# Kernel tuning notes

Hardware: AMD Instinct MI355X
Metric: run time of the kernel (lower is better)

Reference implementation:

```python
import jax, jax.numpy as jnp
import numpy as np
from jax import lax

B, T, F = 8, 512, 128          # batch, mel time, mel freq
DM, DS, DC, EXP, NL = 384, 16, 4, 2, 12
DI = EXP * DM                   # 768 inner width
DTR = (DM + 15) // 16           # 24, mamba_ssm dt_rank='auto'
PT = PF = 16
L = (T // PT) * (F // PF)       # 256 patches
NC = 4


def setup_inputs() -> dict:
    key = jax.random.key(0)
    ks = iter(jax.random.split(key, 24))
    def n(shape, s=0.02):
        return jax.random.normal(next(ks), shape, jnp.float32) * s
    return {
        "x": jax.random.normal(next(ks), (B, T, F), jnp.float32),
        "patch_w": n((DM, PT, PF)),
        "patch_b": jnp.zeros((DM,), jnp.float32),
        "pos_embed": n((1, L, DM)),
        "ln_g": jnp.ones((NL, DM), jnp.float32),
        "ln_b": jnp.zeros((NL, DM), jnp.float32),
        "in_proj_w": n((NL, 2 * DI, DM)),
        "conv_w": n((NL, DI, DC), 0.1),
        "conv_b": jnp.zeros((NL, DI), jnp.float32),
        "x_proj_w": n((NL, DTR + 2 * DS, DI)),
        "dt_proj_w": n((NL, DI, DTR), 0.1),
        "dt_proj_b": n((NL, DI), 0.1),
        "A_log": jnp.tile(jnp.log(jnp.arange(1, DS + 1, dtype=jnp.float32))[None, None, :], (NL, DI, 1)),
        "Dskip": jnp.ones((NL, DI), jnp.float32),
        "out_proj_w": n((NL, DM, DI)),
        "fn_g": jnp.ones((DM,), jnp.float32),
        "fn_b": jnp.zeros((DM,), jnp.float32),
        "head_w": n((NC, DM)),
        "head_b": jnp.zeros((NC,), jnp.float32),
    }


def _layernorm(x, g, b):
    m = x.mean(-1, keepdims=True)
    v = jnp.var(x, axis=-1, keepdims=True)
    return (x - m) * lax.rsqrt(v + 1e-5) * g + b


def _silu(v):
    return v * jax.nn.sigmoid(v)


def _mamba_block(x, p):
    # x: [B, L, DM]; residual Mamba block (pre-LN, dropout=identity in eval)
    ln_g, ln_b, Wi, cw, cb, Wx, Wdt, bdt, A_log, Dsk, Wo = p
    res = x
    h = _layernorm(x, ln_g, ln_b)
    xz = jnp.einsum('bld,ed->ble', h, Wi)          # [B,L,2*DI]
    u, z = jnp.split(xz, 2, axis=-1)
    # causal depthwise conv1d, kernel DC (small, unrolled)
    up = jnp.pad(u, ((0, 0), (DC - 1, 0), (0, 0)))
    u = sum(up[:, k:k + L, :] * cw[:, k] for k in range(DC)) + cb
    u = _silu(u)
    proj = jnp.einsum('bld,ed->ble', u, Wx)        # [B,L,DTR+2*DS]
    dt, Bm, Cm = jnp.split(proj, [DTR, DTR + DS], axis=-1)
    delta = jax.nn.softplus(jnp.einsum('blr,dr->bld', dt, Wdt) + bdt)  # [B,L,DI]
    A = -jnp.exp(A_log)                            # [DI, DS]
    dA = jnp.exp(delta[..., None] * A)             # [B,L,DI,DS]
    dBu = (delta * u)[..., None] * Bm[:, :, None, :]

    def step(hst, inp):
        dA_t, dBu_t, C_t = inp
        hst = dA_t * hst + dBu_t                   # [B,DI,DS]
        return hst, jnp.einsum('bdn,bn->bd', hst, C_t)

    h0 = jnp.zeros((x.shape[0], DI, DS), x.dtype)
    _, ys = lax.scan(step, h0, (dA.swapaxes(0, 1), dBu.swapaxes(0, 1), Cm.swapaxes(0, 1)))
    y = ys.swapaxes(0, 1) + u * Dsk                # [B,L,DI]
    y = y * _silu(z)
    return res + jnp.einsum('bld,ed->ble', y, Wo)


def reference(x, patch_w, patch_b, pos_embed, ln_g, ln_b, in_proj_w, conv_w, conv_b,
              x_proj_w, dt_proj_w, dt_proj_b, A_log, Dskip, out_proj_w,
              fn_g, fn_b, head_w, head_b):
    Bn = x.shape[0]
    # patch embed = non-overlapping 16x16 conv == blocked reshape + einsum
    patches = x.reshape(Bn, T // PT, PT, F // PF, PF)
    tok = jnp.einsum('bhpwq,dpq->bhwd', patches, patch_w) + patch_b
    tok = tok.reshape(Bn, L, DM) + pos_embed

    def layer(carry, p):
        return _mamba_block(carry, p), None

    tok, _ = lax.scan(layer, tok, (ln_g, ln_b, in_proj_w, conv_w, conv_b,
                                   x_proj_w, dt_proj_w, dt_proj_b, A_log, Dskip, out_proj_w))
    tok = _layernorm(tok, fn_g, fn_b)
    pooled = tok.mean(axis=1)
    return pooled @ head_w.T + head_b
```

## Files before the change

kernel.cpp:

```cpp
#include <hip/hip_runtime.h>
#include <math.h>

namespace {

constexpr int kB   = 8;
constexpr int kL   = 256;
constexpr int kTok = 2048;
constexpr int kDM  = 384;
constexpr int kDI  = 768;
constexpr int kDS  = 16;
constexpr int kDTR = 24;
constexpr int kPROJ = 56;
constexpr int kNL  = 12;

constexpr int kWIN  = 2 * kDI * kDM;
constexpr int kWOUT = kDM * kDI;
constexpr int kWX   = kPROJ * kDI;
constexpr int kWTOT = kWIN + kWOUT + kWX;

typedef float f32x4 __attribute__((ext_vector_type(4)));
typedef short short8 __attribute__((ext_vector_type(8)));

__device__ __forceinline__ float softplus_f(float x) {
  return (x > 20.f) ? x : log1pf(__expf(x));
}
__device__ __forceinline__ float silu_f(float x) {
  return x / (1.f + __expf(-x));
}
__device__ __forceinline__ unsigned short f2bf(float f) {
  union { float f; unsigned u; } v; v.f = f;
  unsigned r = v.u + 0x7FFFu + ((v.u >> 16) & 1u);
  return (unsigned short)(r >> 16);
}
__device__ __forceinline__ float bf2f(unsigned short u) {
  return __uint_as_float((unsigned)u << 16);
}

__global__ __launch_bounds__(256) void patch_gemm_k(
    const float* __restrict__ x, const float* __restrict__ Bw,
    const float* __restrict__ bias, const float* __restrict__ pos,
    float* __restrict__ C) {
  __shared__ float As[16][68];
  __shared__ float Bs[16][68];
  int tid = threadIdx.x;
  int bm = blockIdx.y * 64;
  int bn = blockIdx.x * 64;
  int lr = tid >> 2;
  int lk = (tid & 3) << 2;
  int tm = (tid >> 4) << 2;
  int tn = (tid & 15) << 2;
  float acc[4][4] = {};
  for (int k0 = 0; k0 < 256; k0 += 16) {
    {
      int token = bm + lr;
      int b = token >> 8, l = token & 255;
      int h = l >> 3, w = l & 7;
      int p = k0 >> 4;
      const float* ap = x + ((size_t)(b * 512) + h * 16 + p) * 128 + w * 16 + lk;
      float4 av = *(const float4*)ap;
      As[lk + 0][lr] = av.x; As[lk + 1][lr] = av.y;
      As[lk + 2][lr] = av.z; As[lk + 3][lr] = av.w;
    }
    {
      const float* bp = Bw + (size_t)(bn + lr) * 256 + k0 + lk;
      float4 bv = *(const float4*)bp;
      Bs[lk + 0][lr] = bv.x; Bs[lk + 1][lr] = bv.y;
      Bs[lk + 2][lr] = bv.z; Bs[lk + 3][lr] = bv.w;
    }
    __syncthreads();
    #pragma unroll
    for (int k = 0; k < 16; ++k) {
      float4 a = *(const float4*)&As[k][tm];
      float4 b = *(const float4*)&Bs[k][tn];
      float av[4] = {a.x, a.y, a.z, a.w};
      float bv[4] = {b.x, b.y, b.z, b.w};
      #pragma unroll
      for (int i = 0; i < 4; ++i)
        #pragma unroll
        for (int j = 0; j < 4; ++j)
          acc[i][j] = fmaf(av[i], bv[j], acc[i][j]);
    }
    __syncthreads();
  }
  #pragma unroll
  for (int i = 0; i < 4; ++i) {
    int row = bm + tm + i;
    #pragma unroll
    for (int j = 0; j < 4; ++j) {
      int col = bn + tn + j;
      C[(size_t)row * kDM + col] =
          acc[i][j] + bias[col] + pos[(size_t)(row & 255) * kDM + col];
    }
  }
}

__global__ __launch_bounds__(384) void lnpool_k(
    const float* __restrict__ in, float* __restrict__ pooled,
    const float* __restrict__ g, const float* __restrict__ bb) {
  int t = blockIdx.x, d = threadIdx.x;
  float v = in[(size_t)t * kDM + d];
  float s = v, s2 = v * v;
  #pragma unroll
  for (int m = 32; m >= 1; m >>= 1) {
    s  += __shfl_xor(s, m);
    s2 += __shfl_xor(s2, m);
  }
  __shared__ float ps[6], ps2[6];
  if ((d & 63) == 0) { ps[d >> 6] = s; ps2[d >> 6] = s2; }
  __syncthreads();
  float S = 0.f, S2 = 0.f;
  #pragma unroll
  for (int i = 0; i < 6; ++i) { S += ps[i]; S2 += ps2[i]; }
  float mean = S * (1.f / 384.f);
  float var  = S2 * (1.f / 384.f) - mean * mean;
  float r = rsqrtf(var + 1e-5f);
  float o = (v - mean) * r * g[d] + bb[d];
  atomicAdd(&pooled[(size_t)(t >> 8) * kDM + d], o * (1.f / 256.f));
}

__global__ __launch_bounds__(256) void convert_all_k(
    const float* __restrict__ w_in, const float* __restrict__ w_out,
    const float* __restrict__ w_x, unsigned short* __restrict__ dst,
    float* __restrict__ pooled_zero) {
  int layer = blockIdx.y;
  int tid = threadIdx.x;
  if (layer == 0 && blockIdx.x == 0) {
    for (int i = tid; i < kB * kDM; i += 256) pooled_zero[i] = 0.f;
  }
  int i4 = (blockIdx.x * 256 + tid) * 4;
  if (i4 >= kWTOT) return;
  const float* src;
  int off;
  if (i4 < kWIN) { src = w_in + (size_t)layer * kWIN; off = i4; }
  else if (i4 < kWIN + kWOUT) { src = w_out + (size_t)layer * kWOUT; off = i4 - kWIN; }
  else { src = w_x + (size_t)layer * kWX; off = i4 - kWIN - kWOUT; }
  float4 v = *(const float4*)(src + off);
  unsigned short o[4] = {f2bf(v.x), f2bf(v.y), f2bf(v.z), f2bf(v.w)};
  *(uint2*)(dst + (size_t)layer * kWTOT + i4) = *(const uint2*)o;
}

__global__ __launch_bounds__(256) void inproj_ln_k(
    const float* __restrict__ tok, const unsigned short* __restrict__ Bw,
    const float* __restrict__ g, const float* __restrict__ bb,
    unsigned short* __restrict__ Cbf, float* __restrict__ proj_zero) {
  __shared__ __align__(16) unsigned short As[4][64][8];
  __shared__ __align__(16) unsigned short Bs[4][128][8];
  __shared__ float smean[64], srstd[64];
  __shared__ float sg_[kDM], sb_[kDM];
  int tid = threadIdx.x;
  int bm = blockIdx.y * 64;
  int bn = blockIdx.x * 128;
  {
    int bid = blockIdx.y * 12 + blockIdx.x;
    for (int i = bid * 256 + tid; i < kTok * kPROJ; i += 384 * 256)
      proj_zero[i] = 0.f;
  }
  for (int i = tid; i < kDM; i += 256) { sg_[i] = g[i]; sb_[i] = bb[i]; }
  {
    int r = tid >> 2, quarter = tid & 3;
    const float* rp = tok + (size_t)(bm + r) * kDM + quarter * 96;
    float s = 0.f, s2 = 0.f;
    #pragma unroll
    for (int q = 0; q < 24; ++q) {
      float4 v = ((const float4*)rp)[q];
      s  += v.x + v.y + v.z + v.w;
      s2 += v.x * v.x + v.y * v.y + v.z * v.z + v.w * v.w;
    }
    s  += __shfl_xor(s, 1);  s2 += __shfl_xor(s2, 1);
    s  += __shfl_xor(s, 2);  s2 += __shfl_xor(s2, 2);
    if (quarter == 0) {
      float mean = s * (1.f / 384.f);
      float var  = s2 * (1.f / 384.f) - mean * mean;
      smean[r] = mean;
      srstd[r] = rsqrtf(var + 1e-5f);
    }
  }
  __syncthreads();
  int wave = tid >> 6, lane = tid & 63;
  int lm = lane & 15, lq = lane >> 4;
  int wm = (wave & 1) * 32, wn = (wave >> 1) * 64;
  f32x4 acc[2][4] = {};
  for (int k0 = 0; k0 < kDM; k0 += 32) {
    int ar = tid & 63, aq = tid >> 6;
    unsigned short av[8];
    {
      float mean = smean[ar], rstd = srstd[ar];
      const float* ap = tok + (size_t)(bm + ar) * kDM + k0 + aq * 8;
      float4 v0 = ((const float4*)ap)[0];
      float4 v1 = ((const float4*)ap)[1];
      float vv[8] = {v0.x, v0.y, v0.z, v0.w, v1.x, v1.y, v1.z, v1.w};
      #pragma unroll
      for (int j = 0; j < 8; ++j) {
        int k = k0 + aq * 8 + j;
        av[j] = f2bf((vv[j] - mean) * rstd * sg_[k] + sb_[k]);
      }
    }
    int br = tid & 127, bq0 = tid >> 7, bq1 = bq0 + 2;
    uint4 b0 = *(const uint4*)(Bw + (size_t)(bn + br) * kDM + k0 + bq0 * 8);
    uint4 b1 = *(const uint4*)(Bw + (size_t)(bn + br) * kDM + k0 + bq1 * 8);
    __syncthreads();
    *(uint4*)&As[aq][ar][0]  = *(const uint4*)av;
    *(uint4*)&Bs[bq0][br][0] = b0;
    *(uint4*)&Bs[bq1][br][0] = b1;
    __syncthreads();
    short8 bfrag[4];
    #pragma unroll
    for (int ni = 0; ni < 4; ++ni)
      bfrag[ni] = *(const short8*)&Bs[lq][wn + ni * 16 + lm][0];
    #pragma unroll
    for (int mi = 0; mi < 2; ++mi) {
      short8 afrag = *(const short8*)&As[lq][wm + mi * 16 + lm][0];
      #pragma unroll
      for (int ni = 0; ni < 4; ++ni)
        acc[mi][ni] = __builtin_amdgcn_mfma_f32_16x16x32_bf16(
            afrag, bfrag[ni], acc[mi][ni], 0, 0, 0);
    }
  }
  #pragma unroll
  for (int mi = 0; mi < 2; ++mi) {
    #pragma unroll
    for (int ni = 0; ni < 4; ++ni) {
      int grow0 = bm + wm + mi * 16 + lq * 4;
      int gcol = bn + wn + ni * 16 + lm;
      #pragma unroll
      for (int r = 0; r < 4; ++r)
        Cbf[(size_t)(grow0 + r) * (2 * kDI) + gcol] = f2bf(acc[mi][ni][r]);
    }
  }
}

__global__ __launch_bounds__(256) void xproj_conv_k(
    const unsigned short* __restrict__ xz, const unsigned short* __restrict__ Bw,
    const float* __restrict__ cw, const float* __restrict__ cb,
    float* __restrict__ proj, unsigned short* __restrict__ uT_bf,
    unsigned short* __restrict__ sgT_bf) {
  __shared__ __align__(16) unsigned short As[4][64][8];
  __shared__ __align__(16) unsigned short Bs[4][64][8];
  __shared__ float scw[128][4];
  __shared__ float scb[128];
  int tid = threadIdx.x;
  int bm = blockIdx.x * 64;
  int kbase = blockIdx.y * 128;
  int wave = tid >> 6, lane = tid & 63;
  int lm = lane & 15, lq = lane >> 4;
  int wm = wave * 16;
  f32x4 acc[4] = {};

  if (tid < 128) {
    *(float4*)&scw[tid][0] = *(const float4*)(cw + (size_t)(kbase + tid) * 4);
    scb[tid] = cb[kbase + tid];
  }
  __syncthreads();

  int ar = tid & 63;
  int aq = tid >> 6;
  int t = bm + ar;
  int b = t >> 8, l = t & 255;

  for (int kt = 0; kt < 4; ++kt) {
    int k0 = kbase + kt * 32;
    int dloc = kt * 32 + aq * 8;
    int dg = kbase + dloc;
    unsigned short av[8];
    {
      float vals[4][8];
      #pragma unroll
      for (int q = 0; q < 4; ++q) {
        if (l - 3 + q >= 0) {
          uint4 r = *(const uint4*)(xz + (size_t)(t - 3 + q) * (2 * kDI) + dg);
          const unsigned short* rs = (const unsigned short*)&r;
          #pragma unroll
          for (int j = 0; j < 8; ++j) vals[q][j] = bf2f(rs[j]);
        } else {
          #pragma unroll
          for (int j = 0; j < 8; ++j) vals[q][j] = 0.f;
        }
      }
      uint4 zr = *(const uint4*)(xz + (size_t)t * (2 * kDI) + kDI + dg);
      const unsigned short* zs = (const unsigned short*)&zr;
      #pragma unroll
      for (int j = 0; j < 8; ++j) {
        float a = scb[dloc + j];
        a = fmaf(vals[0][j], scw[dloc + j][0], a);
        a = fmaf(vals[1][j], scw[dloc + j][1], a);
        a = fmaf(vals[2][j], scw[dloc + j][2], a);
        a = fmaf(vals[3][j], scw[dloc + j][3], a);
        unsigned short ub = f2bf(silu_f(a));
        av[j] = ub;
        size_t rbase = ((size_t)b * kDI + dg + j) * kL + l;
        uT_bf[rbase] = ub;
        sgT_bf[rbase] = f2bf(silu_f(bf2f(zs[j])));
      }
    }
    int br = tid & 63, bq = tid >> 6;
    uint4 b0;
    if (br < kPROJ)
      b0 = *(const uint4*)(Bw + (size_t)br * kDI + k0 + bq * 8);
    else
      b0 = make_uint4(0u, 0u, 0u, 0u);
    __syncthreads();
    *(uint4*)&As[aq][ar][0] = *(const uint4*)av;
    *(uint4*)&Bs[bq][br][0] = b0;
    __syncthreads();
    short8 afrag = *(const short8*)&As[lq][wm + lm][0];
    #pragma unroll
    for (int ni = 0; ni < 4; ++ni) {
      short8 bfrag = *(const short8*)&Bs[lq][ni * 16 + lm][0];
      acc[ni] = __builtin_amdgcn_mfma_f32_16x16x32_bf16(
          afrag, bfrag, acc[ni], 0, 0, 0);
    }
  }

  #pragma unroll
  for (int ni = 0; ni < 4; ++ni) {
    int grow0 = bm + wm + lq * 4;
    int gcol = ni * 16 + lm;
    if (gcol < kPROJ) {
      #pragma unroll
      for (int r = 0; r < 4; ++r)
        atomicAdd(&proj[(size_t)(grow0 + r) * kPROJ + gcol], acc[ni][r]);
    }
  }
}

__global__ __launch_bounds__(256) void bgemm_out_k(
    const unsigned short* __restrict__ A, int lda,
    const unsigned short* __restrict__ B, int ldb,
    float* __restrict__ C, int ldc, int Kc) {
  __shared__ __align__(16) unsigned short As[4][64][8];
  __shared__ __align__(16) unsigned short Bs[4][64][8];
  int tid = threadIdx.x;
  int bm = blockIdx.y * 64;
  int bn = blockIdx.x * 64;
  int k_begin = blockIdx.z * Kc;
  int wave = tid >> 6, lane = tid & 63;
  int lm = lane & 15, lq = lane >> 4;
  int wm = (wave & 1) * 32, wn = (wave >> 1) * 32;
  f32x4 acc[2][2] = {};

  for (int kt = 0; kt < Kc; kt += 32) {
    int k0 = k_begin + kt;
    int ar = tid & 63, aq = tid >> 6;
    uint4 a0 = *(const uint4*)(A + (size_t)(bm + ar) * lda + k0 + aq * 8);
    uint4 b0 = *(const uint4*)(B + (size_t)(bn + ar) * ldb + k0 + aq * 8);
    __syncthreads();
    *(uint4*)&As[aq][ar][0] = a0;
    *(uint4*)&Bs[aq][ar][0] = b0;
    __syncthreads();
    short8 bfrag[2];
    #pragma unroll
    for (int ni = 0; ni < 2; ++ni)
      bfrag[ni] = *(const short8*)&Bs[lq][wn + ni * 16 + lm][0];
    #pragma unroll
    for (int mi = 0; mi < 2; ++mi) {
      short8 afrag = *(const short8*)&As[lq][wm + mi * 16 + lm][0];
      #pragma unroll
      for (int ni = 0; ni < 2; ++ni)
        acc[mi][ni] = __builtin_amdgcn_mfma_f32_16x16x32_bf16(
            afrag, bfrag[ni], acc[mi][ni], 0, 0, 0);
    }
  }

  #pragma unroll
  for (int mi = 0; mi < 2; ++mi) {
    #pragma unroll
    for (int ni = 0; ni < 2; ++ni) {
      int grow0 = bm + wm + mi * 16 + lq * 4;
      int gcol = bn + wn + ni * 16 + lm;
      #pragma unroll
      for (int r = 0; r < 4; ++r)
        atomicAdd(&C[(size_t)(grow0 + r) * ldc + gcol], acc[mi][ni][r]);
    }
  }
}

__global__ __launch_bounds__(256, 3) void scansplit_k(
    const float* __restrict__ proj, const unsigned short* __restrict__ uT_bf,
    const unsigned short* __restrict__ sgT_bf, const float* __restrict__ dtw,
    const float* __restrict__ dtb, const float* __restrict__ A_log,
    const float* __restrict__ Dsk, unsigned short* __restrict__ y_bf) {
  int d0 = blockIdx.x * 4;
  int b = blockIdx.y;
  int tid = threadIdx.x;
  int dsub = tid & 3;
  int nq = (tid >> 2) & 3;
  int c = tid >> 4;
  int d = d0 + dsub;
  __shared__ float sproj[256][33];
  __shared__ float sdt[16][16][5];
  __shared__ float sh[16][16][5];
  __shared__ float sca[16][16][5];

  const float* pr0 = proj + (size_t)(b * kL) * kPROJ;

  {
    const float* rp = pr0 + (size_t)tid * kPROJ;
    #pragma unroll
    for (int q = 0; q < 6; ++q) {
      float4 v = ((const float4*)rp)[q];
      sproj[tid][q * 4 + 0] = v.x;
      sproj[tid][q * 4 + 1] = v.y;
      sproj[tid][q * 4 + 2] = v.z;
      sproj[tid][q * 4 + 3] = v.w;
    }
  }

  float Av2[4];
  {
    const float kLog2e = 1.44269504088896340736f;
    float4 v = *(const float4*)(A_log + (size_t)d * kDS + nq * 4);
    Av2[0] = -__expf(v.x) * kLog2e;
    Av2[1] = -__expf(v.y) * kLog2e;
    Av2[2] = -__expf(v.z) * kLog2e;
    Av2[3] = -__expf(v.w) * kLog2e;
  }
  float bdt = dtb[d];
  float Dv = Dsk[d];

  float wdt[24];
  {
    const float* wp = dtw + (size_t)d * kDTR;
    #pragma unroll
    for (int q = 0; q < 6; ++q) {
      float4 v = ((const float4*)wp)[q];
      wdt[q * 4 + 0] = v.x; wdt[q * 4 + 1] = v.y;
      wdt[q * 4 + 2] = v.z; wdt[q * 4 + 3] = v.w;
    }
  }

  union { uint4 v[2]; unsigned short s[16]; } uu;
  {
    const unsigned short* up = uT_bf + ((size_t)b * kDI + d) * kL + c * 16;
    uu.v[0] = ((const uint4*)up)[0];
    uu.v[1] = ((const uint4*)up)[1];
  }

  __syncthreads();

  #pragma unroll
  for (int i = 0; i < 4; ++i) {
    int tok = c * 16 + nq * 4 + i;
    float acc = bdt;
    #pragma unroll
    for (int r = 0; r < 24; ++r) acc = fmaf(sproj[tok][r], wdt[r], acc);
    sdt[c][nq * 4 + i][dsub] = softplus_f(acc);
  }
  __syncthreads();

  {
    const float* rp = pr0 + (size_t)tid * kPROJ + 24;
    #pragma unroll
    for (int q = 0; q < 8; ++q) {
      float4 v = ((const float4*)rp)[q];
      sproj[tid][q * 4 + 0] = v.x;
      sproj[tid][q * 4 + 1] = v.y;
      sproj[tid][q * 4 + 2] = v.z;
      sproj[tid][q * 4 + 3] = v.w;
    }
  }
  __syncthreads();

  float h[4] = {};
  float S = 0.f;
  #pragma unroll
  for (int i = 0; i < 16; ++i) {
    int tok = c * 16 + i;
    float dl = sdt[c][i][dsub];
    float du = dl * bf2f(uu.s[i]);
    S += dl;
    #pragma unroll
    for (int n = 0; n < 4; ++n) {
      float a = exp2f(dl * Av2[n]);
      h[n] = fmaf(a, h[n], du * sproj[tok][nq * 4 + n]);
    }
  }
  {
    int nrow = nq * 4;
    #pragma unroll
    for (int n = 0; n < 4; ++n) {
      sh[c][nrow + n][dsub] = h[n];
      sca[c][nrow + n][dsub] = exp2f(S * Av2[n]);
    }
  }
  __syncthreads();

  float h0[4] = {};
  {
    int nrow = nq * 4;
    for (int j = 0; j < c; ++j) {
      #pragma unroll
      for (int n = 0; n < 4; ++n)
        h0[n] = fmaf(sca[j][nrow + n][dsub], h0[n], sh[j][nrow + n][dsub]);
    }
  }

  union { uint4 v[2]; unsigned short s[16]; } zz;
  zz.v[0] = make_uint4(0u, 0u, 0u, 0u);
  zz.v[1] = make_uint4(0u, 0u, 0u, 0u);
  if (nq == 0) {
    const unsigned short* sp = sgT_bf + ((size_t)b * kDI + d) * kL + c * 16;
    zz.v[0] = ((const uint4*)sp)[0];
    zz.v[1] = ((const uint4*)sp)[1];
  }

  unsigned short* yp = y_bf + (size_t)(b * kL + c * 16) * kDI + d;
  #pragma unroll
  for (int i = 0; i < 16; ++i) {
    int tok = c * 16 + i;
    float dl = sdt[c][i][dsub];
    float uv = bf2f(uu.s[i]);
    float du = dl * uv;
    float yv = 0.f;
    #pragma unroll
    for (int n = 0; n < 4; ++n) {
      float a = exp2f(dl * Av2[n]);
      h0[n] = fmaf(a, h0[n], du * sproj[tok][nq * 4 + n]);
      yv = fmaf(h0[n], sproj[tok][16 + nq * 4 + n], yv);
    }
    yv += __shfl_xor(yv, 4);
    yv += __shfl_xor(yv, 8);
    if (nq == 0) yp[(size_t)i * kDI] = f2bf((yv + uv * Dv) * bf2f(zz.s[i]));
  }
}

__global__ __launch_bounds__(64) void head_k(
    const float* __restrict__ pooled, const float* __restrict__ hw,
    const float* __restrict__ hb, float* __restrict__ out) {
  int b = blockIdx.x >> 2, c = blockIdx.x & 3;
  int lane = threadIdx.x;
  float acc = 0.f;
  for (int dd = lane; dd < kDM; dd += 64)
    acc = fmaf(pooled[b * kDM + dd], hw[c * kDM + dd], acc);
  #pragma unroll
  for (int m = 32; m >= 1; m >>= 1) acc += __shfl_xor(acc, m);
  if (lane == 0) out[b * 4 + c] = acc + hb[c];
}

}

extern "C" void kernel_launch(void* const* d_in, const int* in_sizes, int n_in,
                              void* d_out, int out_size, void* d_ws, size_t ws_size,
                              hipStream_t stream) {
  (void)in_sizes; (void)n_in; (void)out_size; (void)ws_size;
  const float* x        = (const float*)d_in[0];
  const float* patch_w  = (const float*)d_in[1];
  const float* patch_b  = (const float*)d_in[2];
  const float* pos      = (const float*)d_in[3];
  const float* ln_g     = (const float*)d_in[4];
  const float* ln_b     = (const float*)d_in[5];
  const float* in_w     = (const float*)d_in[6];
  const float* conv_w   = (const float*)d_in[7];
  const float* conv_b   = (const float*)d_in[8];
  const float* xproj_w  = (const float*)d_in[9];
  const float* dtproj_w = (const float*)d_in[10];
  const float* dtproj_b = (const float*)d_in[11];
  const float* A_log    = (const float*)d_in[12];
  const float* Dskip    = (const float*)d_in[13];
  const float* out_w    = (const float*)d_in[14];
  const float* fn_g     = (const float*)d_in[15];
  const float* fn_b     = (const float*)d_in[16];
  const float* head_w   = (const float*)d_in[17];
  const float* head_b   = (const float*)d_in[18];
  float* out = (float*)d_out;

  float* ws = (float*)d_ws;
  float* tok    = ws; ws += kTok * kDM;
  float* proj   = ws; ws += kTok * kPROJ;
  float* pooled = ws; ws += kB * kDM;
  unsigned short* xz_bf  = (unsigned short*)ws; ws += kTok * 2 * kDI / 2;
  unsigned short* uT_bf  = (unsigned short*)ws; ws += kTok * kDI / 2;
  unsigned short* sgT_bf = (unsigned short*)ws; ws += kTok * kDI / 2;
  unsigned short* y_bf   = (unsigned short*)ws; ws += kTok * kDI / 2;
  unsigned short* w_bf   = (unsigned short*)ws; ws += (size_t)kNL * kWTOT / 2;

  convert_all_k<<<dim3(kWTOT / 4 / 256, kNL), 256, 0, stream>>>(
      in_w, out_w, xproj_w, w_bf, pooled);

  patch_gemm_k<<<dim3(6, 32), 256, 0, stream>>>(x, patch_w, patch_b, pos, tok);

  for (int layer = 0; layer < kNL; ++layer) {
    const unsigned short* wl = w_bf + (size_t)layer * kWTOT;
    inproj_ln_k<<<dim3(12, 32), 256, 0, stream>>>(
        tok, wl, ln_g + layer * kDM, ln_b + layer * kDM, xz_bf, proj);
    xproj_conv_k<<<dim3(32, 6), 256, 0, stream>>>(
        xz_bf, wl + kWIN + kWOUT, conv_w + layer * kDI * 4,
        conv_b + layer * kDI, proj, uT_bf, sgT_bf);
    scansplit_k<<<dim3(kDI / 4, kB), 256, 0, stream>>>(
        proj, uT_bf, sgT_bf, dtproj_w + (size_t)layer * kDI * kDTR,
        dtproj_b + layer * kDI, A_log + (size_t)layer * kDI * kDS,
        Dskip + layer * kDI, y_bf);
    bgemm_out_k<<<dim3(6, 32, 4), 256, 0, stream>>>(
        y_bf, kDI, wl + kWIN, kDI, tok, kDM, kDI / 4);
  }

  lnpool_k<<<kTok, kDM, 0, stream>>>(tok, pooled, fn_g, fn_b);
  head_k<<<kB * 4, 64, 0, stream>>>(pooled, head_w, head_b, out);
}
```

Before: 1.164 ms.

## Fuse all layers into one persistent kernel with software grid barriers

Replaces the roughly fifty per-layer kernel launches with a single persistent mega kernel sized to two blocks per CU. Blocks loop over work units for each stage and synchronise through an atomic counter grid barrier. The in-projection tile also changes from 128 to 96 columns to produce more work units. This is meant to remove launch overhead and inter-kernel gaps, at the cost of barrier spin time, reduced occupancy from the shared 48KB scratch, and a deadlock risk if not all blocks are co-resident.

```diff
diff --git a/kernel.cpp b/kernel.cpp
--- a/kernel.cpp
+++ b/kernel.cpp
@@ -36,96 +36,27 @@
   return __uint_as_float((unsigned)u << 16);
 }
 
-__global__ __launch_bounds__(256) void patch_gemm_k(
-    const float* __restrict__ x, const float* __restrict__ Bw,
-    const float* __restrict__ bias, const float* __restrict__ pos,
-    float* __restrict__ C) {
-  __shared__ float As[16][68];
-  __shared__ float Bs[16][68];
-  int tid = threadIdx.x;
-  int bm = blockIdx.y * 64;
-  int bn = blockIdx.x * 64;
-  int lr = tid >> 2;
-  int lk = (tid & 3) << 2;
-  int tm = (tid >> 4) << 2;
-  int tn = (tid & 15) << 2;
-  float acc[4][4] = {};
-  for (int k0 = 0; k0 < 256; k0 += 16) {
-    {
-      int token = bm + lr;
-      int b = token >> 8, l = token & 255;
-      int h = l >> 3, w = l & 7;
-      int p = k0 >> 4;
-      const float* ap = x + ((size_t)(b * 512) + h * 16 + p) * 128 + w * 16 + lk;
-      float4 av = *(const float4*)ap;
-      As[lk + 0][lr] = av.x; As[lk + 1][lr] = av.y;
-      As[lk + 2][lr] = av.z; As[lk + 3][lr] = av.w;
-    }
-    {
-      const float* bp = Bw + (size_t)(bn + lr) * 256 + k0 + lk;
-      float4 bv = *(const float4*)bp;
-      Bs[lk + 0][lr] = bv.x; Bs[lk + 1][lr] = bv.y;
-      Bs[lk + 2][lr] = bv.z; Bs[lk + 3][lr] = bv.w;
-    }
-    __syncthreads();
-    #pragma unroll
-    for (int k = 0; k < 16; ++k) {
-      float4 a = *(const float4*)&As[k][tm];
-      float4 b = *(const float4*)&Bs[k][tn];
-      float av[4] = {a.x, a.y, a.z, a.w};
-      float bv[4] = {b.x, b.y, b.z, b.w};
-      #pragma unroll
-      for (int i = 0; i < 4; ++i)
-        #pragma unroll
-        for (int j = 0; j < 4; ++j)
-          acc[i][j] = fmaf(av[i], bv[j], acc[i][j]);
-    }
-    __syncthreads();
+__device__ __forceinline__ void gbar(unsigned* cnt, unsigned target) {
+  __syncthreads();
+  if (threadIdx.x == 0) {
+    __builtin_amdgcn_fence(__ATOMIC_SEQ_CST, "agent");
+    __hip_atomic_fetch_add(cnt, 1u, __ATOMIC_RELAXED, __HIP_MEMORY_SCOPE_AGENT);
+    while (__hip_atomic_load(cnt, __ATOMIC_RELAXED, __HIP_MEMORY_SCOPE_AGENT) < target)
+      __builtin_amdgcn_s_sleep(2);
+    __builtin_amdgcn_fence(__ATOMIC_SEQ_CST, "agent");
   }
-  #pragma unroll
-  for (int i = 0; i < 4; ++i) {
-    int row = bm + tm + i;
-    #pragma unroll
-    for (int j = 0; j < 4; ++j) {
-      int col = bn + tn + j;
-      C[(size_t)row * kDM + col] =
-          acc[i][j] + bias[col] + pos[(size_t)(row & 255) * kDM + col];
-    }
-  }
-}
-
-__global__ __launch_bounds__(384) void lnpool_k(
-    const float* __restrict__ in, float* __restrict__ pooled,
-    const float* __restrict__ g, const float* __restrict__ bb) {
-  int t = blockIdx.x, d = threadIdx.x;
-  float v = in[(size_t)t * kDM + d];
-  float s = v, s2 = v * v;
-  #pragma unroll
-  for (int m = 32; m >= 1; m >>= 1) {
-    s  += __shfl_xor(s, m);
-    s2 += __shfl_xor(s2, m);
-  }
-  __shared__ float ps[6], ps2[6];
-  if ((d & 63) == 0) { ps[d >> 6] = s; ps2[d >> 6] = s2; }
   __syncthreads();
-  float S = 0.f, S2 = 0.f;
-  #pragma unroll
-  for (int i = 0; i < 6; ++i) { S += ps[i]; S2 += ps2[i]; }
-  float mean = S * (1.f / 384.f);
-  float var  = S2 * (1.f / 384.f) - mean * mean;
-  float r = rsqrtf(var + 1e-5f);
-  float o = (v - mean) * r * g[d] + bb[d];
-  atomicAdd(&pooled[(size_t)(t >> 8) * kDM + d], o * (1.f / 256.f));
 }
 
 __global__ __launch_bounds__(256) void convert_all_k(
     const float* __restrict__ w_in, const float* __restrict__ w_out,
     const float* __restrict__ w_x, unsigned short* __restrict__ dst,
-    float* __restrict__ pooled_zero) {
+    float* __restrict__ pooled_zero, unsigned* __restrict__ bar) {
   int layer = blockIdx.y;
   int tid = threadIdx.x;
   if (layer == 0 && blockIdx.x == 0) {
     for (int i = tid; i < kB * kDM; i += 256) pooled_zero[i] = 0.f;
+    if (tid < 64) bar[tid] = 0u;
   }
   int i4 = (blockIdx.x * 256 + tid) * 4;
   if (i4 >= kWTOT) return;
@@ -139,401 +70,506 @@
   *(uint2*)(dst + (size_t)layer * kWTOT + i4) = *(const uint2*)o;
 }
 
-__global__ __launch_bounds__(256) void inproj_ln_k(
-    const float* __restrict__ tok, const unsigned short* __restrict__ Bw,
-    const float* __restrict__ g, const float* __restrict__ bb,
-    unsigned short* __restrict__ Cbf, float* __restrict__ proj_zero) {
-  __shared__ __align__(16) unsigned short As[4][64][8];
-  __shared__ __align__(16) unsigned short Bs[4][128][8];
-  __shared__ float smean[64], srstd[64];
-  __shared__ float sg_[kDM], sb_[kDM];
-  int tid = threadIdx.x;
-  int bm = blockIdx.y * 64;
-  int bn = blockIdx.x * 128;
+__global__ __launch_bounds__(256, 2) void mega_k(
+    const float* __restrict__ x, const float* __restrict__ patch_w,
+    const float* __restrict__ patch_b, const float* __restrict__ pos,
+    float* __restrict__ tok,
+    const float* __restrict__ ln_g, const float* __restrict__ ln_b,
+    const unsigned short* __restrict__ w_bf,
+    const float* __restrict__ conv_w, const float* __restrict__ conv_b,
+    const float* __restrict__ dtw_all, const float* __restrict__ dtb_all,
+    const float* __restrict__ Alog_all, const float* __restrict__ Dsk_all,
+    float* __restrict__ proj, unsigned short* __restrict__ xz_bf,
+    unsigned short* __restrict__ uT_bf, unsigned short* __restrict__ sgT_bf,
+    unsigned short* __restrict__ y_bf,
+    const float* __restrict__ fn_g, const float* __restrict__ fn_b,
+    const float* __restrict__ head_w, const float* __restrict__ head_b,
+    float* __restrict__ pooled, float* __restrict__ out,
+    unsigned* __restrict__ bar, int nblk) {
+  __shared__ __align__(16) char smem[49152];
+  const int tid = threadIdx.x;
+  const int bid = blockIdx.x;
+  const int wave = tid >> 6, lane = tid & 63;
+  unsigned bt = 0;
+
   {
-    int bid = blockIdx.y * 12 + blockIdx.x;
-    for (int i = bid * 256 + tid; i < kTok * kPROJ; i += 384 * 256)
-      proj_zero[i] = 0.f;
+    float (*As)[68] = (float(*)[68])smem;
+    float (*Bs)[68] = (float(*)[68])(smem + 4352);
+    for (int u = bid; u < 192; u += nblk) {
+      __syncthreads();
+      int bm = (u / 6) * 64;
+      int bn = (u % 6) * 64;
+      int lr = tid >> 2;
+      int lk = (tid & 3) << 2;
+      int tm = (tid >> 4) << 2;
+      int tn = (tid & 15) << 2;
+      float acc[4][4] = {};
+      for (int k0 = 0; k0 < 256; k0 += 16) {
+        {
+          int token = bm + lr;
+          int b = token >> 8, l = token & 255;
+          int h = l >> 3, w = l & 7;
+          int p = k0 >> 4;
+          const float* ap = x + ((size_t)(b * 512) + h * 16 + p) * 128 + w * 16 + lk;
+          float4 av = *(const float4*)ap;
+          As[lk + 0][lr] = av.x; As[lk + 1][lr] = av.y;
+          As[lk + 2][lr] = av.z; As[lk + 3][lr] = av.w;
+        }
+        {
+          const float* bp = patch_w + (size_t)(bn + lr) * 256 + k0 + lk;
+          float4 bv = *(const float4*)bp;
+          Bs[lk + 0][lr] = bv.x; Bs[lk + 1][lr] = bv.y;
+          Bs[lk + 2][lr] = bv.z; Bs[lk + 3][lr] = bv.w;
+        }
+        __syncthreads();
+        #pragma unroll
+        for (int k = 0; k < 16; ++k) {
+          float4 a = *(const float4*)&As[k][tm];
+          float4 b = *(const float4*)&Bs[k][tn];
+          float av[4] = {a.x, a.y, a.z, a.w};
+          float bv[4] = {b.x, b.y, b.z, b.w};
+          #pragma unroll
+          for (int i = 0; i < 4; ++i)
+            #pragma unroll
+            for (int j = 0; j < 4; ++j)
+              acc[i][j] = fmaf(av[i], bv[j], acc[i][j]);
+        }
+        __syncthreads();
+      }
+      #pragma unroll
+      for (int i = 0; i < 4; ++i) {
+        int row = bm + tm + i;
+        #pragma unroll
+        for (int j = 0; j < 4; ++j) {
+          int col = bn + tn + j;
+          tok[(size_t)row * kDM + col] =
+              acc[i][j] + patch_b[col] + pos[(size_t)(row & 255) * kDM + col];
+        }
+      }
+    }
   }
-  for (int i = tid; i < kDM; i += 256) { sg_[i] = g[i]; sb_[i] = bb[i]; }
+  gbar(bar, bt += (unsigned)nblk);
+
+  for (int layer = 0; layer < kNL; ++layer) {
+    const unsigned short* wl = w_bf + (size_t)layer * kWTOT;
+
+    {
+      for (int i = bid * 256 + tid; i < kTok * kPROJ; i += nblk * 256)
+        proj[i] = 0.f;
+      float* sg_ = (float*)smem;
+      float* sb_ = (float*)(smem + 1536);
+      float* smean = (float*)(smem + 3072);
+      float* srstd = (float*)(smem + 3328);
+      auto As = (unsigned short (*)[64][8])(smem + 3584);
+      auto Bs = (unsigned short (*)[96][8])(smem + 7680);
+      const float* g = ln_g + (size_t)layer * kDM;
+      const float* bbp = ln_b + (size_t)layer * kDM;
+      for (int u = bid; u < 512; u += nblk) {
+        __syncthreads();
+        int bm = (u >> 4) * 64;
+        int bn = (u & 15) * 96;
+        for (int i = tid; i < kDM; i += 256) { sg_[i] = g[i]; sb_[i] = bbp[i]; }
+        {
+          int r = tid >> 2, quarter = tid & 3;
+          const float* rp = tok + (size_t)(bm + r) * kDM + quarter * 96;
+          float s = 0.f, s2 = 0.f;
+          #pragma unroll
+          for (int q = 0; q < 24; ++q) {
+            float4 v = ((const float4*)rp)[q];
+            s  += v.x + v.y + v.z + v.w;
+            s2 += v.x * v.x + v.y * v.y + v.z * v.z + v.w * v.w;
+          }
+          s  += __shfl_xor(s, 1);  s2 += __shfl_xor(s2, 1);
+          s  += __shfl_xor(s, 2);  s2 += __shfl_xor(s2, 2);
+          if (quarter == 0) {
+            float mean = s * (1.f / 384.f);
+            float var  = s2 * (1.f / 384.f) - mean * mean;
+            smean[r] = mean;
+            srstd[r] = rsqrtf(var + 1e-5f);
+          }
+        }
+        __syncthreads();
+        int lm = lane & 15, lq = lane >> 4;
+        int wm = (wave & 1) * 32, wn = (wave >> 1) * 48;
+        int ar = tid & 63, aq = tid >> 6;
+        int r0 = tid >> 2, q0 = tid & 3;
+        int r1 = (tid + 256) >> 2;
+        f32x4 acc[2][3] = {};
+        for (int k0 = 0; k0 < kDM; k0 += 32) {
+          unsigned short av[8];
+          {
+            float mean = smean[ar], rstd = srstd[ar];
+            const float* ap = tok + (size_t)(bm + ar) * kDM + k0 + aq * 8;
+            float4 v0 = ((const float4*)ap)[0];
+            float4 v1 = ((const float4*)ap)[1];
+            float vv[8] = {v0.x, v0.y, v0.z, v0.w, v1.x, v1.y, v1.z, v1.w};
+            #pragma unroll
+            for (int j = 0; j < 8; ++j) {
+              int k = k0 + aq * 8 + j;
+              av[j] = f2bf((vv[j] - mean) * rstd * sg_[k] + sb_[k]);
+            }
+          }
+          uint4 bv0 = *(const uint4*)(wl + (size_t)(bn + r0) * kDM + k0 + q0 * 8);
+          uint4 bv1 = make_uint4(0u, 0u, 0u, 0u);
+          if (tid < 128)
+            bv1 = *(const uint4*)(wl + (size_t)(bn + r1) * kDM + k0 + q0 * 8);
+          __syncthreads();
+          *(uint4*)&As[aq][ar][0] = *(const uint4*)av;
+          *(uint4*)&Bs[q0][r0][0] = bv0;
+          if (tid < 128) *(uint4*)&Bs[q0][r1][0] = bv1;
+          __syncthreads();
+          short8 bfrag[3];
+          #pragma unroll
+          for (int ni = 0; ni < 3; ++ni)
+            bfrag[ni] = *(const short8*)&Bs[lq][wn + ni * 16 + lm][0];
+          #pragma unroll
+          for (int mi = 0; mi < 2; ++mi) {
+            short8 afrag = *(const short8*)&As[lq][wm + mi * 16 + lm][0];
+            #pragma unroll
+            for (int ni = 0; ni < 3; ++ni)
+              acc[mi][ni] = __builtin_amdgcn_mfma_f32_16x16x32_bf16(
+                  afrag, bfrag[ni], acc[mi][ni], 0, 0, 0);
+          }
+        }
+        #pragma unroll
+        for (int mi = 0; mi < 2; ++mi) {
+          #pragma unroll
+          for (int ni = 0; ni < 3; ++ni) {
+            int grow0 = bm + wm + mi * 16 + lq * 4;
+            int gcol = bn + wn + ni * 16 + lm;
+            #pragma unroll
+            for (int r = 0; r < 4; ++r)
+              xz_bf[(size_t)(grow0 + r) * (2 * kDI) + gcol] = f2bf(acc[mi][ni][r]);
+          }
+        }
+      }
+    }
+    gbar(bar, bt += (unsigned)nblk);
+
+    {
+      auto As = (unsigned short (*)[64][8])smem;
+      auto Bs = (unsigned short (*)[64][8])(smem + 4096);
+      auto scw = (float (*)[4])(smem + 8192);
+      float* scb = (float*)(smem + 10240);
+      const float* cw = conv_w + (size_t)layer * kDI * 4;
+      const float* cb = conv_b + (size_t)layer * kDI;
+      const unsigned short* Bw = wl + kWIN + kWOUT;
+      for (int u = bid; u < 192; u += nblk) {
+        __syncthreads();
+        int bm = (u & 31) * 64;
+        int kbase = (u >> 5) * 128;
+        int lm = lane & 15, lq = lane >> 4;
+        int wm = wave * 16;
+        f32x4 acc[4] = {};
+        if (tid < 128) {
+          *(float4*)&scw[tid][0] = *(const float4*)(cw + (size_t)(kbase + tid) * 4);
+          scb[tid] = cb[kbase + tid];
+        }
+        __syncthreads();
+        int ar = tid & 63;
+        int aq = tid >> 6;
+        int t = bm + ar;
+        int b = t >> 8, l = t & 255;
+        for (int kt = 0; kt < 4; ++kt) {
+          int k0 = kbase + kt * 32;
+          int dloc = kt * 32 + aq * 8;
+          int dg = kbase + dloc;
+          unsigned short av[8];
+          {
+            float vals[4][8];
+            #pragma unroll
+            for (int q = 0; q < 4; ++q) {
+              if (l - 3 + q >= 0) {
+                uint4 r = *(const uint4*)(xz_bf + (size_t)(t - 3 + q) * (2 * kDI) + dg);
+                const unsigned short* rs = (const unsigned short*)&r;
+                #pragma unroll
+                for (int j = 0; j < 8; ++j) vals[q][j] = bf2f(rs[j]);
+              } else {
+                #pragma unroll
+                for (int j = 0; j < 8; ++j) vals[q][j] = 0.f;
+              }
+            }
+            uint4 zr = *(const uint4*)(xz_bf + (size_t)t * (2 * kDI) + kDI + dg);
+            const unsigned short* zs = (const unsigned short*)&zr;
+            #pragma unroll
+            for (int j = 0; j < 8; ++j) {
+              float a = scb[dloc + j];
+              a = fmaf(vals[0][j], scw[dloc + j][0], a);
+              a = fmaf(vals[1][j], scw[dloc + j][1], a);
+              a = fmaf(vals[2][j], scw[dloc + j][2], a);
+              a = fmaf(vals[3][j], scw[dloc + j][3], a);
+              unsigned short ub = f2bf(silu_f(a));
+              av[j] = ub;
+              size_t rbase = ((size_t)b * kDI + dg + j) * kL + l;
+              uT_bf[rbase] = ub;
+              sgT_bf[rbase] = f2bf(silu_f(bf2f(zs[j])));
+            }
+          }
+          int br = tid & 63, bq = tid >> 6;
+          uint4 b0;
+          if (br < kPROJ)
+            b0 = *(const uint4*)(Bw + (size_t)br * kDI + k0 + bq * 8);
+          else
+            b0 = make_uint4(0u, 0u, 0u, 0u);
+          __syncthreads();
+          *(uint4*)&As[aq][ar][0] = *(const uint4*)av;
+          *(uint4*)&Bs[bq][br][0] = b0;
+          __syncthreads();
+          short8 afrag = *(const short8*)&As[lq][wm + lm][0];
+          #pragma unroll
+          for (int ni = 0; ni < 4; ++ni) {
+            short8 bfrag = *(const short8*)&Bs[lq][ni * 16 + lm][0];
+            acc[ni] = __builtin_amdgcn_mfma_f32_16x16x32_bf16(
+                afrag, bfrag, acc[ni], 0, 0, 0);
+          }
+        }
+        #pragma unroll
+        for (int ni = 0; ni < 4; ++ni) {
+          int grow0 = bm + wm + lq * 4;
+          int gcol = ni * 16 + lm;
+          if (gcol < kPROJ) {
+            #pragma unroll
+            for (int r = 0; r < 4; ++r)
+              atomicAdd(&proj[(size_t)(grow0 + r) * kPROJ + gcol], acc[ni][r]);
+          }
+        }
+      }
+    }
+    gbar(bar, bt += (unsigned)nblk);
+
+    {
+      float (*sproj)[33] = (float(*)[33])smem;
+      auto sdt = (float (*)[16][5])(smem + 33792);
+      auto sh  = (float (*)[16][5])(smem + 38912);
+      auto sca = (float (*)[16][5])(smem + 44032);
+      const float* dtw = dtw_all + (size_t)layer * kDI * kDTR;
+      const float* dtb = dtb_all + (size_t)layer * kDI;
+      const float* Alog = Alog_all + (size_t)layer * kDI * kDS;
+      const float* Dskp = Dsk_all + (size_t)layer * kDI;
+      int dsub = tid & 3;
+      int nq = (tid >> 2) & 3;
+      int c = tid >> 4;
+      for (int u = bid; u < 1536; u += nblk) {
+        __syncthreads();
+        int d0 = (u % 192) * 4;
+        int b = u / 192;
+        int d = d0 + dsub;
+        const float* pr0 = proj + (size_t)(b * kL) * kPROJ;
+        {
+          const float* rp = pr0 + (size_t)tid * kPROJ;
+          #pragma unroll
+          for (int q = 0; q < 6; ++q) {
+            float4 v = ((const float4*)rp)[q];
+            sproj[tid][q * 4 + 0] = v.x;
+            sproj[tid][q * 4 + 1] = v.y;
+            sproj[tid][q * 4 + 2] = v.z;
+            sproj[tid][q * 4 + 3] = v.w;
+          }
+        }
+        float Av2[4];
+        {
+          const float kLog2e = 1.44269504088896340736f;
+          float4 v = *(const float4*)(Alog + (size_t)d * kDS + nq * 4);
+          Av2[0] = -__expf(v.x) * kLog2e;
+          Av2[1] = -__expf(v.y) * kLog2e;
+          Av2[2] = -__expf(v.z) * kLog2e;
+          Av2[3] = -__expf(v.w) * kLog2e;
+        }
+        float bdt = dtb[d];
+        float Dv = Dskp[d];
+        float wdt[24];
+        {
+          const float* wp = dtw + (size_t)d * kDTR;
+          #pragma unroll
+          for (int q = 0; q < 6; ++q) {
+            float4 v = ((const float4*)wp)[q];
+            wdt[q * 4 + 0] = v.x; wdt[q * 4 + 1] = v.y;
+            wdt[q * 4 + 2] = v.z; wdt[q * 4 + 3] = v.w;
+          }
+        }
+        union { uint4 v[2]; unsigned short s[16]; } uu;
+        {
+          const unsigned short* up = uT_bf + ((size_t)b * kDI + d) * kL + c * 16;
+          uu.v[0] = ((const uint4*)up)[0];
+          uu.v[1] = ((const uint4*)up)[1];
+        }
+        __syncthreads();
+        #pragma unroll
+        for (int i = 0; i < 4; ++i) {
+          int tk = c * 16 + nq * 4 + i;
+          float acc = bdt;
+          #pragma unroll
+          for (int r = 0; r < 24; ++r) acc = fmaf(sproj[tk][r], wdt[r], acc);
+          sdt[c][nq * 4 + i][dsub] = softplus_f(acc);
+        }
+        __syncthreads();
+        {
+          const float* rp = pr0 + (size_t)tid * kPROJ + 24;
+          #pragma unroll
+          for (int q = 0; q < 8; ++q) {
+            float4 v = ((const float4*)rp)[q];
+            sproj[tid][q * 4 + 0] = v.x;
+            sproj[tid][q * 4 + 1] = v.y;
+            sproj[tid][q * 4 + 2] = v.z;
+            sproj[tid][q * 4 + 3] = v.w;
+          }
+        }
+        __syncthreads();
+        float h[4] = {};
+        float S = 0.f;
+        #pragma unroll
+        for (int i = 0; i < 16; ++i) {
+          int tk = c * 16 + i;
+          float dl = sdt[c][i][dsub];
+          float du = dl * bf2f(uu.s[i]);
+          S += dl;
+          #pragma unroll
+          for (int n = 0; n < 4; ++n) {
+            float a = exp2f(dl * Av2[n]);
+            h[n] = fmaf(a, h[n], du * sproj[tk][nq * 4 + n]);
+          }
+        }
+        {
+          int nrow = nq * 4;
+          #pragma unroll
+          for (int n = 0; n < 4; ++n) {
+            sh[c][nrow + n][dsub] = h[n];
+            sca[c][nrow + n][dsub] = exp2f(S * Av2[n]);
+          }
+        }
+        __syncthreads();
+        float h0[4] = {};
+        {
+          int nrow = nq * 4;
+          for (int j = 0; j < c; ++j) {
+            #pragma unroll
+            for (int n = 0; n < 4; ++n)
+              h0[n] = fmaf(sca[j][nrow + n][dsub], h0[n], sh[j][nrow + n][dsub]);
+          }
+        }
+        union { uint4 v[2]; unsigned short s[16]; } zz;
+        zz.v[0] = make_uint4(0u, 0u, 0u, 0u);
+        zz.v[1] = make_uint4(0u, 0u, 0u, 0u);
+        if (nq == 0) {
+          const unsigned short* sp = sgT_bf + ((size_t)b * kDI + d) * kL + c * 16;
+          zz.v[0] = ((const uint4*)sp)[0];
+          zz.v[1] = ((const uint4*)sp)[1];
+        }
+        unsigned short* yp = y_bf + (size_t)(b * kL + c * 16) * kDI + d;
+        #pragma unroll
+        for (int i = 0; i < 16; ++i) {
+          int tk = c * 16 + i;
+          float dl = sdt[c][i][dsub];
+          float uv = bf2f(uu.s[i]);
+          float du = dl * uv;
+          float yv = 0.f;
+          #pragma unroll
+          for (int n = 0; n < 4; ++n) {
+            float a = exp2f(dl * Av2[n]);
+            h0[n] = fmaf(a, h0[n], du * sproj[tk][nq * 4 + n]);
+            yv = fmaf(h0[n], sproj[tk][16 + nq * 4 + n], yv);
+          }
+          yv += __shfl_xor(yv, 4);
+          yv += __shfl_xor(yv, 8);
+          if (nq == 0) yp[(size_t)i * kDI] = f2bf((yv + uv * Dv) * bf2f(zz.s[i]));
+        }
+      }
+    }
+    gbar(bar, bt += (unsigned)nblk);
+
+    {
+      auto As = (unsigned short (*)[64][8])smem;
+      auto Bs = (unsigned short (*)[64][8])(smem + 4096);
+      const unsigned short* Bw = wl + kWIN;
+      for (int u = bid; u < 768; u += nblk) {
+        __syncthreads();
+        int bn = (u % 6) * 64;
+        int bm = ((u / 6) & 31) * 64;
+        int k_begin = (u / 192) * 192;
+        int lm = lane & 15, lq = lane >> 4;
+        int wm = (wave & 1) * 32, wn = (wave >> 1) * 32;
+        f32x4 acc[2][2] = {};
+        for (int kt = 0; kt < 192; kt += 32) {
+          int k0 = k_begin + kt;
+          int ar = tid & 63, aq = tid >> 6;
+          uint4 a0 = *(const uint4*)(y_bf + (size_t)(bm + ar) * kDI + k0 + aq * 8);
+          uint4 b0 = *(const uint4*)(Bw + (size_t)(bn + ar) * kDI + k0 + aq * 8);
+          __syncthreads();
+          *(uint4*)&As[aq][ar][0] = a0;
+          *(uint4*)&Bs[aq][ar][0] = b0;
+          __syncthreads();
+          short8 bfrag[2];
+          #pragma unroll
+          for (int ni = 0; ni < 2; ++ni)
+            bfrag[ni] = *(const short8*)&Bs[lq][wn + ni * 16 + lm][0];
+          #pragma unroll
+          for (int mi = 0; mi < 2; ++mi) {
+            short8 afrag = *(const short8*)&As[lq][wm + mi * 16 + lm][0];
+            #pragma unroll
+            for (int ni = 0; ni < 2; ++ni)
+              acc[mi][ni] = __builtin_amdgcn_mfma_f32_16x16x32_bf16(
+                  afrag, bfrag[ni], acc[mi][ni], 0, 0, 0);
+          }
+        }
+        #pragma unroll
+        for (int mi = 0; mi < 2; ++mi) {
+          #pragma unroll
+          for (int ni = 0; ni < 2; ++ni) {
+            int grow0 = bm + wm + mi * 16 + lq * 4;
+            int gcol = bn + wn + ni * 16 + lm;
+            #pragma unroll
+            for (int r = 0; r < 4; ++r)
+              atomicAdd(&tok[(size_t)(grow0 + r) * kDM + gcol], acc[mi][ni][r]);
+          }
+        }
+      }
+    }
+    gbar(bar, bt += (unsigned)nblk);
+  }
+
   {
-    int r = tid >> 2, quarter = tid & 3;
-    const float* rp = tok + (size_t)(bm + r) * kDM + quarter * 96;
-    float s = 0.f, s2 = 0.f;
-    #pragma unroll
-    for (int q = 0; q < 24; ++q) {
-      float4 v = ((const float4*)rp)[q];
-      s  += v.x + v.y + v.z + v.w;
-      s2 += v.x * v.x + v.y * v.y + v.z * v.z + v.w * v.w;
-    }
-    s  += __shfl_xor(s, 1);  s2 += __shfl_xor(s2, 1);
-    s  += __shfl_xor(s, 2);  s2 += __shfl_xor(s2, 2);
-    if (quarter == 0) {
+    for (int t = bid * 4 + wave; t < kTok; t += nblk * 4) {
+      float v[6];
+      float s = 0.f, s2 = 0.f;
+      #pragma unroll
+      for (int j = 0; j < 6; ++j) {
+        int d = lane + j * 64;
+        v[j] = tok[(size_t)t * kDM + d];
+        s += v[j];
+        s2 += v[j] * v[j];
+      }
+      #pragma unroll
+      for (int m = 32; m >= 1; m >>= 1) {
+        s  += __shfl_xor(s, m);
+        s2 += __shfl_xor(s2, m);
+      }
       float mean = s * (1.f / 384.f);
       float var  = s2 * (1.f / 384.f) - mean * mean;
-      smean[r] = mean;
-      srstd[r] = rsqrtf(var + 1e-5f);
+      float r = rsqrtf(var + 1e-5f);
+      #pragma unroll
+      for (int j = 0; j < 6; ++j) {
+        int d = lane + j * 64;
+        float o = (v[j] - mean) * r * fn_g[d] + fn_b[d];
+        atomicAdd(&pooled[(size_t)(t >> 8) * kDM + d], o * (1.f / 256.f));
+      }
     }
   }
-  __syncthreads();
-  int wave = tid >> 6, lane = tid & 63;
-  int lm = lane & 15, lq = lane >> 4;
-  int wm = (wave & 1) * 32, wn = (wave >> 1) * 64;
-  f32x4 acc[2][4] = {};
-  for (int k0 = 0; k0 < kDM; k0 += 32) {
-    int ar = tid & 63, aq = tid >> 6;
-    unsigned short av[8];
-    {
-      float mean = smean[ar], rstd = srstd[ar];
-      const float* ap = tok + (size_t)(bm + ar) * kDM + k0 + aq * 8;
-      float4 v0 = ((const float4*)ap)[0];
-      float4 v1 = ((const float4*)ap)[1];
-      float vv[8] = {v0.x, v0.y, v0.z, v0.w, v1.x, v1.y, v1.z, v1.w};
+  gbar(bar, bt += (unsigned)nblk);
+
+  for (int u = bid; u < kB * 4; u += nblk) {
+    if (wave == 0) {
+      int b = u >> 2, c = u & 3;
+      float acc = 0.f;
       #pragma unroll
-      for (int j = 0; j < 8; ++j) {
-        int k = k0 + aq * 8 + j;
-        av[j] = f2bf((vv[j] - mean) * rstd * sg_[k] + sb_[k]);
-      }
-    }
-    int br = tid & 127, bq0 = tid >> 7, bq1 = bq0 + 2;
-    uint4 b0 = *(const uint4*)(Bw + (size_t)(bn + br) * kDM + k0 + bq0 * 8);
-    uint4 b1 = *(const uint4*)(Bw + (size_t)(bn + br) * kDM + k0 + bq1 * 8);
-    __syncthreads();
-    *(uint4*)&As[aq][ar][0]  = *(const uint4*)av;
-    *(uint4*)&Bs[bq0][br][0] = b0;
-    *(uint4*)&Bs[bq1][br][0] = b1;
-    __syncthreads();
-    short8 bfrag[4];
-    #pragma unroll
-    for (int ni = 0; ni < 4; ++ni)
-      bfrag[ni] = *(const short8*)&Bs[lq][wn + ni * 16 + lm][0];
-    #pragma unroll
-    for (int mi = 0; mi < 2; ++mi) {
-      short8 afrag = *(const short8*)&As[lq][wm + mi * 16 + lm][0];
+      for (int j = 0; j < 6; ++j) {
+        int d = lane + j * 64;
+        acc = fmaf(pooled[(size_t)b * kDM + d], head_w[(size_t)c * kDM + d], acc);
+      }
       #pragma unroll
-      for (int ni = 0; ni < 4; ++ni)
-        acc[mi][ni] = __builtin_amdgcn_mfma_f32_16x16x32_bf16(
-            afrag, bfrag[ni], acc[mi][ni], 0, 0, 0);
+      for (int m = 32; m >= 1; m >>= 1) acc += __shfl_xor(acc, m);
+      if (lane == 0) out[b * 4 + c] = acc + head_b[c];
     }
   }
-  #pragma unroll
-  for (int mi = 0; mi < 2; ++mi) {
-    #pragma unroll
-    for (int ni = 0; ni < 4; ++ni) {
-      int grow0 = bm + wm + mi * 16 + lq * 4;
-      int gcol = bn + wn + ni * 16 + lm;
-      #pragma unroll
-      for (int r = 0; r < 4; ++r)
-        Cbf[(size_t)(grow0 + r) * (2 * kDI) + gcol] = f2bf(acc[mi][ni][r]);
-    }
-  }
-}
-
-__global__ __launch_bounds__(256) void xproj_conv_k(
-    const unsigned short* __restrict__ xz, const unsigned short* __restrict__ Bw,
-    const float* __restrict__ cw, const float* __restrict__ cb,
-    float* __restrict__ proj, unsigned short* __restrict__ uT_bf,
-    unsigned short* __restrict__ sgT_bf) {
-  __shared__ __align__(16) unsigned short As[4][64][8];
-  __shared__ __align__(16) unsigned short Bs[4][64][8];
-  __shared__ float scw[128][4];
-  __shared__ float scb[128];
-  int tid = threadIdx.x;
-  int bm = blockIdx.x * 64;
-  int kbase = blockIdx.y * 128;
-  int wave = tid >> 6, lane = tid & 63;
-  int lm = lane & 15, lq = lane >> 4;
-  int wm = wave * 16;
-  f32x4 acc[4] = {};
-
-  if (tid < 128) {
-    *(float4*)&scw[tid][0] = *(const float4*)(cw + (size_t)(kbase + tid) * 4);
-    scb[tid] = cb[kbase + tid];
-  }
-  __syncthreads();
-
-  int ar = tid & 63;
-  int aq = tid >> 6;
-  int t = bm + ar;
-  int b = t >> 8, l = t & 255;
-
-  for (int kt = 0; kt < 4; ++kt) {
-    int k0 = kbase + kt * 32;
-    int dloc = kt * 32 + aq * 8;
-    int dg = kbase + dloc;
-    unsigned short av[8];
-    {
-      float vals[4][8];
-      #pragma unroll
-      for (int q = 0; q < 4; ++q) {
-        if (l - 3 + q >= 0) {
-          uint4 r = *(const uint4*)(xz + (size_t)(t - 3 + q) * (2 * kDI) + dg);
-          const unsigned short* rs = (const unsigned short*)&r;
-          #pragma unroll
-          for (int j = 0; j < 8; ++j) vals[q][j] = bf2f(rs[j]);
-        } else {
-          #pragma unroll
-          for (int j = 0; j < 8; ++j) vals[q][j] = 0.f;
-        }
-      }
-      uint4 zr = *(const uint4*)(xz + (size_t)t * (2 * kDI) + kDI + dg);
-      const unsigned short* zs = (const unsigned short*)&zr;
-      #pragma unroll
-      for (int j = 0; j < 8; ++j) {
-        float a = scb[dloc + j];
-        a = fmaf(vals[0][j], scw[dloc + j][0], a);
-        a = fmaf(vals[1][j], scw[dloc + j][1], a);
-        a = fmaf(vals[2][j], scw[dloc + j][2], a);
-        a = fmaf(vals[3][j], scw[dloc + j][3], a);
-        unsigned short ub = f2bf(silu_f(a));
-        av[j] = ub;
-        size_t rbase = ((size_t)b * kDI + dg + j) * kL + l;
-        uT_bf[rbase] = ub;
-        sgT_bf[rbase] = f2bf(silu_f(bf2f(zs[j])));
-      }
-    }
-    int br = tid & 63, bq = tid >> 6;
-    uint4 b0;
-    if (br < kPROJ)
-      b0 = *(const uint4*)(Bw + (size_t)br * kDI + k0 + bq * 8);
-    else
-      b0 = make_uint4(0u, 0u, 0u, 0u);
-    __syncthreads();
-    *(uint4*)&As[aq][ar][0] = *(const uint4*)av;
-    *(uint4*)&Bs[bq][br][0] = b0;
-    __syncthreads();
-    short8 afrag = *(const short8*)&As[lq][wm + lm][0];
-    #pragma unroll
-    for (int ni = 0; ni < 4; ++ni) {
-      short8 bfrag = *(const short8*)&Bs[lq][ni * 16 + lm][0];
-      acc[ni] = __builtin_amdgcn_mfma_f32_16x16x32_bf16(
-          afrag, bfrag, acc[ni], 0, 0, 0);
-    }
-  }
-
-  #pragma unroll
-  for (int ni = 0; ni < 4; ++ni) {
-    int grow0 = bm + wm + lq * 4;
-    int gcol = ni * 16 + lm;
-    if (gcol < kPROJ) {
-      #pragma unroll
-      for (int r = 0; r < 4; ++r)
-        atomicAdd(&proj[(size_t)(grow0 + r) * kPROJ + gcol], acc[ni][r]);
-    }
-  }
-}
-
-__global__ __launch_bounds__(256) void bgemm_out_k(
-    const unsigned short* __restrict__ A, int lda,
-    const unsigned short* __restrict__ B, int ldb,
-    float* __restrict__ C, int ldc, int Kc) {
-  __shared__ __align__(16) unsigned short As[4][64][8];
-  __shared__ __align__(16) unsigned short Bs[4][64][8];
-  int tid = threadIdx.x;
-  int bm = blockIdx.y * 64;
-  int bn = blockIdx.x * 64;
-  int k_begin = blockIdx.z * Kc;
-  int wave = tid >> 6, lane = tid & 63;
-  int lm = lane & 15, lq = lane >> 4;
-  int wm = (wave & 1) * 32, wn = (wave >> 1) * 32;
-  f32x4 acc[2][2] = {};
-
-  for (int kt = 0; kt < Kc; kt += 32) {
-    int k0 = k_begin + kt;
-    int ar = tid & 63, aq = tid >> 6;
-    uint4 a0 = *(const uint4*)(A + (size_t)(bm + ar) * lda + k0 + aq * 8);
-    uint4 b0 = *(const uint4*)(B + (size_t)(bn + ar) * ldb + k0 + aq * 8);
-    __syncthreads();
-    *(uint4*)&As[aq][ar][0] = a0;
-    *(uint4*)&Bs[aq][ar][0] = b0;
-    __syncthreads();
-    short8 bfrag[2];
-    #pragma unroll
-    for (int ni = 0; ni < 2; ++ni)
-      bfrag[ni] = *(const short8*)&Bs[lq][wn + ni * 16 + lm][0];
-    #pragma unroll
-    for (int mi = 0; mi < 2; ++mi) {
-      short8 afrag = *(const short8*)&As[lq][wm + mi * 16 + lm][0];
-      #pragma unroll
-      for (int ni = 0; ni < 2; ++ni)
-        acc[mi][ni] = __builtin_amdgcn_mfma_f32_16x16x32_bf16(
-            afrag, bfrag[ni], acc[mi][ni], 0, 0, 0);
-    }
-  }
-
-  #pragma unroll
-  for (int mi = 0; mi < 2; ++mi) {
-    #pragma unroll
-    for (int ni = 0; ni < 2; ++ni) {
-      int grow0 = bm + wm + mi * 16 + lq * 4;
-      int gcol = bn + wn + ni * 16 + lm;
-      #pragma unroll
-      for (int r = 0; r < 4; ++r)
-        atomicAdd(&C[(size_t)(grow0 + r) * ldc + gcol], acc[mi][ni][r]);
-    }
-  }
-}
-
-__global__ __launch_bounds__(256, 3) void scansplit_k(
-    const float* __restrict__ proj, const unsigned short* __restrict__ uT_bf,
-    const unsigned short* __restrict__ sgT_bf, const float* __restrict__ dtw,
-    const float* __restrict__ dtb, const float* __restrict__ A_log,
-    const float* __restrict__ Dsk, unsigned short* __restrict__ y_bf) {
-  int d0 = blockIdx.x * 4;
-  int b = blockIdx.y;
-  int tid = threadIdx.x;
-  int dsub = tid & 3;
-  int nq = (tid >> 2) & 3;
-  int c = tid >> 4;
-  int d = d0 + dsub;
-  __shared__ float sproj[256][33];
-  __shared__ float sdt[16][16][5];
-  __shared__ float sh[16][16][5];
-  __shared__ float sca[16][16][5];
-
-  const float* pr0 = proj + (size_t)(b * kL) * kPROJ;
-
-  {
-    const float* rp = pr0 + (size_t)tid * kPROJ;
-    #pragma unroll
-    for (int q = 0; q < 6; ++q) {
-      float4 v = ((const float4*)rp)[q];
-      sproj[tid][q * 4 + 0] = v.x;
-      sproj[tid][q * 4 + 1] = v.y;
-      sproj[tid][q * 4 + 2] = v.z;
-      sproj[tid][q * 4 + 3] = v.w;
-    }
-  }
-
-  float Av2[4];
-  {
-    const float kLog2e = 1.44269504088896340736f;
-    float4 v = *(const float4*)(A_log + (size_t)d * kDS + nq * 4);
-    Av2[0] = -__expf(v.x) * kLog2e;
-    Av2[1] = -__expf(v.y) * kLog2e;
-    Av2[2] = -__expf(v.z) * kLog2e;
-    Av2[3] = -__expf(v.w) * kLog2e;
-  }
-  float bdt = dtb[d];
-  float Dv = Dsk[d];
-
-  float wdt[24];
-  {
-    const float* wp = dtw + (size_t)d * kDTR;
-    #pragma unroll
-    for (int q = 0; q < 6; ++q) {
-      float4 v = ((const float4*)wp)[q];
-      wdt[q * 4 + 0] = v.x; wdt[q * 4 + 1] = v.y;
-      wdt[q * 4 + 2] = v.z; wdt[q * 4 + 3] = v.w;
-    }
-  }
-
-  union { uint4 v[2]; unsigned short s[16]; } uu;
-  {
-    const unsigned short* up = uT_bf + ((size_t)b * kDI + d) * kL + c * 16;
-    uu.v[0] = ((const uint4*)up)[0];
-    uu.v[1] = ((const uint4*)up)[1];
-  }
-
-  __syncthreads();
-
-  #pragma unroll
-  for (int i = 0; i < 4; ++i) {
-    int tok = c * 16 + nq * 4 + i;
-    float acc = bdt;
-    #pragma unroll
-    for (int r = 0; r < 24; ++r) acc = fmaf(sproj[tok][r], wdt[r], acc);
-    sdt[c][nq * 4 + i][dsub] = softplus_f(acc);
-  }
-  __syncthreads();
-
-  {
-    const float* rp = pr0 + (size_t)tid * kPROJ + 24;
-    #pragma unroll
-    for (int q = 0; q < 8; ++q) {
-      float4 v = ((const float4*)rp)[q];
-      sproj[tid][q * 4 + 0] = v.x;
-      sproj[tid][q * 4 + 1] = v.y;
-      sproj[tid][q * 4 + 2] = v.z;
-      sproj[tid][q * 4 + 3] = v.w;
-    }
-  }
-  __syncthreads();
-
-  float h[4] = {};
-  float S = 0.f;
-  #pragma unroll
-  for (int i = 0; i < 16; ++i) {
-    int tok = c * 16 + i;
-    float dl = sdt[c][i][dsub];
-    float du = dl * bf2f(uu.s[i]);
-    S += dl;
-    #pragma unroll
-    for (int n = 0; n < 4; ++n) {
-      float a = exp2f(dl * Av2[n]);
-      h[n] = fmaf(a, h[n], du * sproj[tok][nq * 4 + n]);
-    }
-  }
-  {
-    int nrow = nq * 4;
-    #pragma unroll
-    for (int n = 0; n < 4; ++n) {
-      sh[c][nrow + n][dsub] = h[n];
-      sca[c][nrow + n][dsub] = exp2f(S * Av2[n]);
-    }
-  }
-  __syncthreads();
-
-  float h0[4] = {};
-  {
-    int nrow = nq * 4;
-    for (int j = 0; j < c; ++j) {
-      #pragma unroll
-      for (int n = 0; n < 4; ++n)
-        h0[n] = fmaf(sca[j][nrow + n][dsub], h0[n], sh[j][nrow + n][dsub]);
-    }
-  }
-
-  union { uint4 v[2]; unsigned short s[16]; } zz;
-  zz.v[0] = make_uint4(0u, 0u, 0u, 0u);
-  zz.v[1] = make_uint4(0u, 0u, 0u, 0u);
-  if (nq == 0) {
-    const unsigned short* sp = sgT_bf + ((size_t)b * kDI + d) * kL + c * 16;
-    zz.v[0] = ((const uint4*)sp)[0];
-    zz.v[1] = ((const uint4*)sp)[1];
-  }
-
-  unsigned short* yp = y_bf + (size_t)(b * kL + c * 16) * kDI + d;
-  #pragma unroll
-  for (int i = 0; i < 16; ++i) {
-    int tok = c * 16 + i;
-    float dl = sdt[c][i][dsub];
-    float uv = bf2f(uu.s[i]);
-    float du = dl * uv;
-    float yv = 0.f;
-    #pragma unroll
-    for (int n = 0; n < 4; ++n) {
-      float a = exp2f(dl * Av2[n]);
-      h0[n] = fmaf(a, h0[n], du * sproj[tok][nq * 4 + n]);
-      yv = fmaf(h0[n], sproj[tok][16 + nq * 4 + n], yv);
-    }
-    yv += __shfl_xor(yv, 4);
-    yv += __shfl_xor(yv, 8);
-    if (nq == 0) yp[(size_t)i * kDI] = f2bf((yv + uv * Dv) * bf2f(zz.s[i]));
-  }
-}
-
-__global__ __launch_bounds__(64) void head_k(
-    const float* __restrict__ pooled, const float* __restrict__ hw,
-    const float* __restrict__ hb, float* __restrict__ out) {
-  int b = blockIdx.x >> 2, c = blockIdx.x & 3;
-  int lane = threadIdx.x;
-  float acc = 0.f;
-  for (int dd = lane; dd < kDM; dd += 64)
-    acc = fmaf(pooled[b * kDM + dd], hw[c * kDM + dd], acc);
-  #pragma unroll
-  for (int m = 32; m >= 1; m >>= 1) acc += __shfl_xor(acc, m);
-  if (lane == 0) out[b * 4 + c] = acc + hb[c];
 }
 
 }
@@ -563,7 +599,17 @@
   const float* head_b   = (const float*)d_in[18];
   float* out = (float*)d_out;
 
+  static int nblk = 0;
+  if (nblk == 0) {
+    hipDeviceProp_t prop;
+    hipGetDeviceProperties(&prop, 0);
+    int b2 = prop.multiProcessorCount * 2;
+    nblk = b2 < 512 ? b2 : 512;
+    if (nblk < 1) nblk = 1;
+  }
+
   float* ws = (float*)d_ws;
+  unsigned* bar = (unsigned*)ws; ws += 64;
   float* tok    = ws; ws += kTok * kDM;
   float* proj   = ws; ws += kTok * kPROJ;
   float* pooled = ws; ws += kB * kDM;
@@ -574,25 +620,10 @@
   unsigned short* w_bf   = (unsigned short*)ws; ws += (size_t)kNL * kWTOT / 2;
 
   convert_all_k<<<dim3(kWTOT / 4 / 256, kNL), 256, 0, stream>>>(
-      in_w, out_w, xproj_w, w_bf, pooled);
-
-  patch_gemm_k<<<dim3(6, 32), 256, 0, stream>>>(x, patch_w, patch_b, pos, tok);
-
-  for (int layer = 0; layer < kNL; ++layer) {
-    const unsigned short* wl = w_bf + (size_t)layer * kWTOT;
-    inproj_ln_k<<<dim3(12, 32), 256, 0, stream>>>(
-        tok, wl, ln_g + layer * kDM, ln_b + layer * kDM, xz_bf, proj);
-    xproj_conv_k<<<dim3(32, 6), 256, 0, stream>>>(
-        xz_bf, wl + kWIN + kWOUT, conv_w + layer * kDI * 4,
-        conv_b + layer * kDI, proj, uT_bf, sgT_bf);
-    scansplit_k<<<dim3(kDI / 4, kB), 256, 0, stream>>>(
-        proj, uT_bf, sgT_bf, dtproj_w + (size_t)layer * kDI * kDTR,
-        dtproj_b + layer * kDI, A_log + (size_t)layer * kDI * kDS,
-        Dskip + layer * kDI, y_bf);
-    bgemm_out_k<<<dim3(6, 32, 4), 256, 0, stream>>>(
-        y_bf, kDI, wl + kWIN, kDI, tok, kDM, kDI / 4);
-  }
-
-  lnpool_k<<<kTok, kDM, 0, stream>>>(tok, pooled, fn_g, fn_b);
-  head_k<<<kB * 4, 64, 0, stream>>>(pooled, head_w, head_b, out);
-}
+      in_w, out_w, xproj_w, w_bf, pooled, bar);
+
+  mega_k<<<nblk, 256, 0, stream>>>(
+      x, patch_w, patch_b, pos, tok, ln_g, ln_b, w_bf, conv_w, conv_b,
+      dtproj_w, dtproj_b, A_log, Dskip, proj, xz_bf, uT_bf, sgT_bf, y_bf,
+      fn_g, fn_b, head_w, head_b, pooled, out, bar, nblk);
+}
```

Measured after the change: 3.613 ms. 3.1x slower.
